# Optimization experiments

Measured on AMD Instinct MI355X. Metric: run time of the kernel, lower is better.

The kernel has to match this reference:

```python
import jax, jax.numpy as jnp
import numpy as np

B, L = 32, 512
H, W = 352, 1216
MAXLEN = max(H, W)  # max Bresenham path length after clipping to image


def setup_inputs() -> dict:
    key = jax.random.key(0)
    k1, k2 = jax.random.split(key)
    pred = jax.random.normal(k1, (B, 1, H, W), dtype=jnp.float32)
    lines = jax.random.randint(k2, (B, L, 2, 2), 0, 1216, dtype=jnp.int32)
    return {"pred": pred, "lines": lines}


def _bresenham_paths(lines):
    # lines: [B, L, 2, 2] int32, last dim = (x, y), coords already clipped.
    # Closed-form skimage/Bresenham: along the major axis i=0..dmaj,
    # minor_i = min0 + smin * floor((2*dmin*i + dmaj) / (2*dmaj)).
    x0 = lines[..., 0, 0]; y0 = lines[..., 0, 1]
    x1 = lines[..., 1, 0]; y1 = lines[..., 1, 1]
    dx = jnp.abs(x1 - x0); dy = jnp.abs(y1 - y0)
    xmajor = dx > dy  # skimage 'steep' swap: x is major iff |dx| > |dy|
    dmaj = jnp.where(xmajor, dx, dy)
    dmin = jnp.where(xmajor, dy, dx)
    smaj = jnp.where(xmajor, jnp.sign(x1 - x0), jnp.sign(y1 - y0))
    smin = jnp.where(xmajor, jnp.sign(y1 - y0), jnp.sign(x1 - x0))
    maj0 = jnp.where(xmajor, x0, y0)
    min0 = jnp.where(xmajor, y0, x0)
    i = jnp.arange(MAXLEN, dtype=jnp.int32)
    # Clamp step index to dmaj -> padding repeats the endpoint, so diffs there are 0.
    i_eff = jnp.minimum(i[None, None, :], dmaj[..., None])       # [B, L, MAXLEN]
    dmaj_e = dmaj[..., None]
    dmaj_safe = jnp.maximum(dmaj_e, 1)
    maj = maj0[..., None] + smaj[..., None] * i_eff
    minr = min0[..., None] + smin[..., None] * (
        (2 * dmin[..., None] * i_eff + dmaj_e) // (2 * dmaj_safe))
    xs = jnp.where(xmajor[..., None], maj, minr)
    ys = jnp.where(xmajor[..., None], minr, maj)
    return xs, ys


def reference(pred, lines):
    # Clip coords into the image, exactly like the torch module.
    x = jnp.clip(lines[..., 0], 0, W - 1)
    y = jnp.clip(lines[..., 1], 0, H - 1)
    lines_c = jnp.stack([x, y], axis=-1)                          # [B, L, 2, 2]

    xs, ys = _bresenham_paths(lines_c)                            # [B, L, MAXLEN]
    p = pred.reshape(B, H * W)
    idx = (ys * W + xs).reshape(B, -1)
    vals = jnp.take_along_axis(p, idx, axis=1).reshape(B, L, MAXLEN)

    # Sum of |diff| of depth along each line (padding repeats endpoint -> 0 diff).
    diff_sums = jnp.sum(jnp.abs(jnp.diff(vals, axis=-1)), axis=-1)  # [B, L]
    # Skip lines whose endpoint depth gap < 0.5 (data-dependent skip -> mask).
    end_diff = jnp.abs(vals[..., 0] - vals[..., -1])
    diff_sums = jnp.where(end_diff < 0.5, 0.0, diff_sums)

    # Angle-based weights (computed from clipped lines, as in the original).
    lf = lines_c.astype(jnp.float32)
    slopes = jnp.abs((lf[:, :, 1, 1] - lf[:, :, 0, 1]) /
                     (lf[:, :, 1, 0] - lf[:, :, 0, 0] + 1e-6))
    degrees = (jnp.arctan(slopes) * 180.0 / jnp.pi) % 90.0
    mx = jnp.max(degrees, axis=1, keepdims=True)                  # per-sample max
    skew_factor = 1.5
    skewed = degrees ** skew_factor / (mx + 1.0) ** (skew_factor - 1.0)
    sharp = 2.5
    heights = 90.0 - (jnp.abs(skewed - 45.0) ** sharp) ** (1.0 / sharp)
    weights = (heights / 300.0) ** 4

    return jnp.sum(weights * diff_sums)
```

## Files before the change

kernel.cpp:

```cpp
#include <hip/hip_runtime.h>
#include <math.h>

#define BB 32
#define LL 512
#define HH 352
#define WW 1216
#define NLINES (BB * LL)
#define LPW 2
#define NBLK2 (NLINES / (LPW * 4))

typedef float f4 __attribute__((ext_vector_type(4), aligned(4)));

__device__ __forceinline__ float line_degree(int x0, int y0, int x1, int y1) {
    float slope = fabsf(((float)y1 - (float)y0) / ((float)x1 - (float)x0 + 1e-6f));
    float deg = (atanf(slope) * 180.0f) / 3.14159274101257324f;
    return fmodf(deg, 90.0f);
}

__device__ __forceinline__ float walk_line(const float* __restrict__ p, int lane,
        int x0, int y0, int x1, int y1, int dy, bool xm, int dmaj, int dmin) {
    float s = 0.0f;
    if (dy == 0) {
        int rb = y0 * WW;
        int xlo = min(x0, x1);
        int dxs = dmaj;
        int PV = dxs & ~3;
        int nch = (PV + 255) >> 8;
        for (int j = 0; j < nch; ++j) {
            int p0 = (j << 8) + (lane << 2);
            bool act = p0 < PV;
            int c = rb + xlo + (act ? p0 : 0);
            f4 lo = *(const f4*)(p + c);
            f4 hi = *(const f4*)(p + c + 1);
            if (act) {
                s += fabsf(hi.x - lo.x) + fabsf(hi.y - lo.y)
                   + fabsf(hi.z - lo.z) + fabsf(hi.w - lo.w);
            }
        }
        if (lane < 3) {
            int i = PV + lane;
            if (i < dxs) {
                float a  = p[rb + xlo + i];
                float bv = p[rb + xlo + i + 1];
                s += fabsf(bv - a);
            }
        }
    } else {
        int sx = (x1 > x0) - (x1 < x0);
        int sy = (y1 > y0) - (y1 < y0);
        int smaj = xm ? sx : sy;
        int smin = xm ? sy : sx;
        int maj0 = xm ? x0 : y0;
        int min0 = xm ? y0 : x0;
        unsigned den = 2u * (unsigned)dmaj;
        int tdm = 2 * dmin;
        unsigned M = 0xFFFFFFFFu / den + 1u;
        int sA = xm ? 1 : WW;
        int sB = xm ? WW : 1;
        int A = smaj * sA;
        int Bm = smin * sB;
        int off0 = maj0 * sA + min0 * sB;
        int niter = (dmaj + 62) / 63;
        int nbatch = (niter + 7) >> 3;
        int idx = lane;
        for (int t = 0; t < nbatch; ++t, idx += 504) {
            int offs[8];
            #pragma unroll
            for (int k = 0; k < 8; ++k) {
                int idc = min(idx + 63 * k, dmaj);
                unsigned num = (unsigned)(tdm * idc) + (unsigned)dmaj;
                unsigned q = __umulhi(num, M);
                q -= (q * den > num) ? 1u : 0u;
                offs[k] = off0 + idc * A + (int)q * Bm;
            }
            float v[8];
            #pragma unroll
            for (int k = 0; k < 8; ++k) v[k] = p[offs[k]];
            #pragma unroll
            for (int k = 0; k < 8; ++k) {
                float vn = __shfl_down(v[k], 1);
                float d = fabsf(vn - v[k]);
                s += (lane < 63) ? d : 0.0f;
            }
        }
    }
    return s;
}

__global__ void __launch_bounds__(256) line_walk_kernel(
        const float* __restrict__ pred, const int* __restrict__ lines,
        float* __restrict__ partials, unsigned* __restrict__ counter) {
    if (blockIdx.x == 0 && threadIdx.x == 0) *counter = 0;
    int lane = threadIdx.x & 63;
    int w = threadIdx.x >> 6;
    int bid = blockIdx.x;
    int swz = (bid & 7) * (NBLK2 / 8) + (bid >> 3);
    int W = swz * 4 + w;
    int g0 = W * LPW, g1 = g0 + 1;
    int b = g0 >> 9;

    int4 lA = ((const int4*)lines)[g0];
    int4 lB = ((const int4*)lines)[g1];
    int ax0 = min(max(lA.x, 0), WW - 1), ay0 = min(max(lA.y, 0), HH - 1);
    int ax1 = min(max(lA.z, 0), WW - 1), ay1 = min(max(lA.w, 0), HH - 1);
    int bx0 = min(max(lB.x, 0), WW - 1), by0 = min(max(lB.y, 0), HH - 1);
    int bx1 = min(max(lB.z, 0), WW - 1), by1 = min(max(lB.w, 0), HH - 1);

    const float* __restrict__ p = pred + (size_t)b * (HH * WW);

    float vfA = p[ay0 * WW + ax0];
    float vlA = p[ay1 * WW + ax1];
    float vfB = p[by0 * WW + bx0];
    float vlB = p[by1 * WW + bx1];

    int adx = abs(ax1 - ax0), ady = abs(ay1 - ay0);
    bool axm = adx > ady;
    int admaj = axm ? adx : ady, admin_ = axm ? ady : adx;
    int bdx = abs(bx1 - bx0), bdy = abs(by1 - by0);
    bool bxm = bdx > bdy;
    int bdmaj = bxm ? bdx : bdy, bdmin = bxm ? bdy : bdx;

    bool actA = (fabsf(vfA - vlA) >= 0.5f) && (admaj > 0);
    bool actB = (fabsf(vfB - vlB) >= 0.5f) && (bdmaj > 0);

    float s0 = actA ? walk_line(p, lane, ax0, ay0, ax1, ay1, ady, axm, admaj, admin_) : 0.0f;
    float s1 = actB ? walk_line(p, lane, bx0, by0, bx1, by1, bdy, bxm, bdmaj, bdmin) : 0.0f;

    #pragma unroll
    for (int off = 32; off > 0; off >>= 1) {
        s0 += __shfl_down(s0, off);
        s1 += __shfl_down(s1, off);
    }
    if (lane == 0) {
        partials[g0] = actA ? s0 : 0.0f;
        partials[g1] = actB ? s1 : 0.0f;
    }
}

__global__ void finalize_kernel(const int* __restrict__ lines,
                                const float* __restrict__ partials,
                                float* __restrict__ bsum,
                                unsigned* __restrict__ counter,
                                float* __restrict__ out) {
    __shared__ float red[LL];
    int b = blockIdx.x;
    int t = threadIdx.x;
    int g = b * LL + t;
    int4 ln = ((const int4*)lines)[g];
    int x0 = min(max(ln.x, 0), WW - 1);
    int y0 = min(max(ln.y, 0), HH - 1);
    int x1 = min(max(ln.z, 0), WW - 1);
    int y1 = min(max(ln.w, 0), HH - 1);
    float deg = line_degree(x0, y0, x1, y1);
    red[t] = deg;
    __syncthreads();
    for (int s = LL / 2; s > 0; s >>= 1) {
        if (t < s) red[t] = fmaxf(red[t], red[t + s]);
        __syncthreads();
    }
    float mxv = red[0];
    __syncthreads();
    float skewed = (deg * sqrtf(deg)) / sqrtf(mxv + 1.0f);
    float tt = fabsf(skewed - 45.0f);
    float h = 90.0f - tt;
    float hw = h * (1.0f / 300.0f);
    float hw2 = hw * hw;
    float wgt = hw2 * hw2;
    red[t] = wgt * partials[g];
    __syncthreads();
    for (int s = LL / 2; s > 0; s >>= 1) {
        if (t < s) red[t] += red[t + s];
        __syncthreads();
    }
    if (t == 0) {
        bsum[b] = red[0];
        __threadfence();
        if (atomicAdd(counter, 1u) == BB - 1) {
            __threadfence();
            float tot = 0.0f;
            #pragma unroll
            for (int i = 0; i < BB; ++i) tot += bsum[i];
            out[0] = tot;
        }
    }
}

extern "C" void kernel_launch(void* const* d_in, const int* in_sizes, int n_in,
                              void* d_out, int out_size, void* d_ws, size_t ws_size,
                              hipStream_t stream) {
    const float* pred = (const float*)d_in[0];
    const int* lines = (const int*)d_in[1];
    float* out = (float*)d_out;
    float* ws = (float*)d_ws;
    float* partials = ws;
    float* bsum = ws + NLINES;
    unsigned* counter = (unsigned*)(ws + NLINES + BB);

    line_walk_kernel<<<NBLK2, 256, 0, stream>>>(pred, lines, partials, counter);
    finalize_kernel<<<BB, LL, 0, stream>>>(lines, partials, bsum, counter, out);
}
```

Baseline: 21.66 us.

## Interleave both lines' gather walks in one loop, drop horizontal vector path

New measurement: 22.92 us. +5.8%, slower.

```diff
diff --git a/kernel.cpp b/kernel.cpp
--- a/kernel.cpp
+++ b/kernel.cpp
@@ -9,82 +9,56 @@
 #define LPW 2
 #define NBLK2 (NLINES / (LPW * 4))
 
-typedef float f4 __attribute__((ext_vector_type(4), aligned(4)));
-
 __device__ __forceinline__ float line_degree(int x0, int y0, int x1, int y1) {
     float slope = fabsf(((float)y1 - (float)y0) / ((float)x1 - (float)x0 + 1e-6f));
     float deg = (atanf(slope) * 180.0f) / 3.14159274101257324f;
     return fmodf(deg, 90.0f);
 }
 
-__device__ __forceinline__ float walk_line(const float* __restrict__ p, int lane,
-        int x0, int y0, int x1, int y1, int dy, bool xm, int dmaj, int dmin) {
-    float s = 0.0f;
-    if (dy == 0) {
-        int rb = y0 * WW;
-        int xlo = min(x0, x1);
-        int dxs = dmaj;
-        int PV = dxs & ~3;
-        int nch = (PV + 255) >> 8;
-        for (int j = 0; j < nch; ++j) {
-            int p0 = (j << 8) + (lane << 2);
-            bool act = p0 < PV;
-            int c = rb + xlo + (act ? p0 : 0);
-            f4 lo = *(const f4*)(p + c);
-            f4 hi = *(const f4*)(p + c + 1);
-            if (act) {
-                s += fabsf(hi.x - lo.x) + fabsf(hi.y - lo.y)
-                   + fabsf(hi.z - lo.z) + fabsf(hi.w - lo.w);
-            }
-        }
-        if (lane < 3) {
-            int i = PV + lane;
-            if (i < dxs) {
-                float a  = p[rb + xlo + i];
-                float bv = p[rb + xlo + i + 1];
-                s += fabsf(bv - a);
-            }
-        }
-    } else {
-        int sx = (x1 > x0) - (x1 < x0);
-        int sy = (y1 > y0) - (y1 < y0);
-        int smaj = xm ? sx : sy;
-        int smin = xm ? sy : sx;
-        int maj0 = xm ? x0 : y0;
-        int min0 = xm ? y0 : x0;
-        unsigned den = 2u * (unsigned)dmaj;
-        int tdm = 2 * dmin;
-        unsigned M = 0xFFFFFFFFu / den + 1u;
-        int sA = xm ? 1 : WW;
-        int sB = xm ? WW : 1;
-        int A = smaj * sA;
-        int Bm = smin * sB;
-        int off0 = maj0 * sA + min0 * sB;
-        int niter = (dmaj + 62) / 63;
-        int nbatch = (niter + 7) >> 3;
-        int idx = lane;
-        for (int t = 0; t < nbatch; ++t, idx += 504) {
-            int offs[8];
-            #pragma unroll
-            for (int k = 0; k < 8; ++k) {
-                int idc = min(idx + 63 * k, dmaj);
-                unsigned num = (unsigned)(tdm * idc) + (unsigned)dmaj;
-                unsigned q = __umulhi(num, M);
-                q -= (q * den > num) ? 1u : 0u;
-                offs[k] = off0 + idc * A + (int)q * Bm;
-            }
-            float v[8];
-            #pragma unroll
-            for (int k = 0; k < 8; ++k) v[k] = p[offs[k]];
-            #pragma unroll
-            for (int k = 0; k < 8; ++k) {
-                float vn = __shfl_down(v[k], 1);
-                float d = fabsf(vn - v[k]);
-                s += (lane < 63) ? d : 0.0f;
-            }
-        }
-    }
-    return s;
+struct Ctx {
+    int off0, A, Bm, tdm;
+    int dmaj;
+    int dwalk;
+    unsigned den, M;
+    int ep0, ep1;
+};
+
+__device__ __forceinline__ Ctx make_ctx(int4 ln) {
+    Ctx c;
+    int x0 = min(max(ln.x, 0), WW - 1);
+    int y0 = min(max(ln.y, 0), HH - 1);
+    int x1 = min(max(ln.z, 0), WW - 1);
+    int y1 = min(max(ln.w, 0), HH - 1);
+    int dx = abs(x1 - x0), dy = abs(y1 - y0);
+    bool xm = dx > dy;
+    c.dmaj = xm ? dx : dy;
+    int dmin = xm ? dy : dx;
+    int sx = (x1 > x0) - (x1 < x0);
+    int sy = (y1 > y0) - (y1 < y0);
+    int smaj = xm ? sx : sy;
+    int smin = xm ? sy : sx;
+    int maj0 = xm ? x0 : y0;
+    int min0 = xm ? y0 : x0;
+    int sA = xm ? 1 : WW;
+    int sB = xm ? WW : 1;
+    c.A = smaj * sA;
+    c.Bm = smin * sB;
+    c.off0 = maj0 * sA + min0 * sB;
+    c.tdm = 2 * dmin;
+    c.den = (unsigned)max(2 * c.dmaj, 2);
+    c.M = 0xFFFFFFFFu / c.den + 1u;
+    c.ep0 = y0 * WW + x0;
+    c.ep1 = y1 * WW + x1;
+    c.dwalk = 0;
+    return c;
+}
+
+__device__ __forceinline__ int path_off(const Ctx& c, int idx) {
+    int idc = min(idx, c.dwalk);
+    unsigned num = (unsigned)(c.tdm * idc) + (unsigned)c.dmaj;
+    unsigned q = __umulhi(num, c.M);
+    q -= (q * c.den > num) ? 1u : 0u;
+    return c.off0 + idc * c.A + (int)q * c.Bm;
 }
 
 __global__ void __launch_bounds__(256) line_walk_kernel(
@@ -101,31 +75,48 @@
 
     int4 lA = ((const int4*)lines)[g0];
     int4 lB = ((const int4*)lines)[g1];
-    int ax0 = min(max(lA.x, 0), WW - 1), ay0 = min(max(lA.y, 0), HH - 1);
-    int ax1 = min(max(lA.z, 0), WW - 1), ay1 = min(max(lA.w, 0), HH - 1);
-    int bx0 = min(max(lB.x, 0), WW - 1), by0 = min(max(lB.y, 0), HH - 1);
-    int bx1 = min(max(lB.z, 0), WW - 1), by1 = min(max(lB.w, 0), HH - 1);
+    Ctx cA = make_ctx(lA);
+    Ctx cB = make_ctx(lB);
 
     const float* __restrict__ p = pred + (size_t)b * (HH * WW);
 
-    float vfA = p[ay0 * WW + ax0];
-    float vlA = p[ay1 * WW + ax1];
-    float vfB = p[by0 * WW + bx0];
-    float vlB = p[by1 * WW + bx1];
+    float vfA = p[cA.ep0];
+    float vlA = p[cA.ep1];
+    float vfB = p[cB.ep0];
+    float vlB = p[cB.ep1];
 
-    int adx = abs(ax1 - ax0), ady = abs(ay1 - ay0);
-    bool axm = adx > ady;
-    int admaj = axm ? adx : ady, admin_ = axm ? ady : adx;
-    int bdx = abs(bx1 - bx0), bdy = abs(by1 - by0);
-    bool bxm = bdx > bdy;
-    int bdmaj = bxm ? bdx : bdy, bdmin = bxm ? bdy : bdx;
+    bool actA = (fabsf(vfA - vlA) >= 0.5f) && (cA.dmaj > 0);
+    bool actB = (fabsf(vfB - vlB) >= 0.5f) && (cB.dmaj > 0);
+    cA.dwalk = actA ? cA.dmaj : 0;
+    cB.dwalk = actB ? cB.dmaj : 0;
 
-    bool actA = (fabsf(vfA - vlA) >= 0.5f) && (admaj > 0);
-    bool actB = (fabsf(vfB - vlB) >= 0.5f) && (bdmaj > 0);
+    int nbA = actA ? ((cA.dmaj + 62) / 63 + 7) >> 3 : 0;
+    int nbB = actB ? ((cB.dmaj + 62) / 63 + 7) >> 3 : 0;
+    int rounds = max(nbA, nbB);
 
-    float s0 = actA ? walk_line(p, lane, ax0, ay0, ax1, ay1, ady, axm, admaj, admin_) : 0.0f;
-    float s1 = actB ? walk_line(p, lane, bx0, by0, bx1, by1, bdy, bxm, bdmaj, bdmin) : 0.0f;
-
+    float s0 = 0.0f, s1 = 0.0f;
+    int idx = lane;
+    for (int t = 0; t < rounds; ++t, idx += 504) {
+        int offsA[8], offsB[8];
+        #pragma unroll
+        for (int k = 0; k < 8; ++k) {
+            offsA[k] = path_off(cA, idx + 63 * k);
+            offsB[k] = path_off(cB, idx + 63 * k);
+        }
+        float vA[8], vB[8];
+        #pragma unroll
+        for (int k = 0; k < 8; ++k) vA[k] = p[offsA[k]];
+        #pragma unroll
+        for (int k = 0; k < 8; ++k) vB[k] = p[offsB[k]];
+        #pragma unroll
+        for (int k = 0; k < 8; ++k) {
+            float nA = __shfl_down(vA[k], 1);
+            float nB = __shfl_down(vB[k], 1);
+            float dA = fabsf(nA - vA[k]);
+            float dB = fabsf(nB - vB[k]);
+            if (lane < 63) { s0 += dA; s1 += dB; }
+        }
+    }
     #pragma unroll
     for (int off = 32; off > 0; off >>= 1) {
         s0 += __shfl_down(s0, off);
```
